# Kernel tuning notes

Hardware: AMD Instinct MI355X
Metric: run time of the kernel (lower is better)

Reference implementation:

```python
import jax, jax.numpy as jnp
import numpy as np

B, L, D, N = 4, 1024, 1024, 16
HD = D // N
DFF = 4 * D
EPS = 1e-5


def _ln(x, g, b):
    m = jnp.mean(x, axis=-1, keepdims=True)
    v = jnp.mean(jnp.square(x - m), axis=-1, keepdims=True)
    return (x - m) * jax.lax.rsqrt(v + EPS) * g + b


def setup_inputs() -> dict:
    key = jax.random.key(0)
    ks = jax.random.split(key, 8)
    s = 0.02
    return {
        "x": jax.random.normal(ks[0], (B, L, D), jnp.float32),
        "decay": jax.random.uniform(ks[1], (N, L, L), jnp.float32),
        "ln1_g": jnp.ones((D,), jnp.float32),
        "ln1_b": jnp.zeros((D,), jnp.float32),
        "proj_W": jax.random.normal(ks[2], (4 * D, D), jnp.float32) * s,
        "proj_b": jnp.zeros((4 * D,), jnp.float32),
        "reto_W": jax.random.normal(ks[3], (D, D), jnp.float32) * s,
        "reto_b": jnp.zeros((D,), jnp.float32),
        "ln2_g": jnp.ones((D,), jnp.float32),
        "ln2_b": jnp.zeros((D,), jnp.float32),
        "ffn1_W": jax.random.normal(ks[4], (DFF, D), jnp.float32) * s,
        "ffn1_b": jnp.zeros((DFF,), jnp.float32),
        "ffn2_W": jax.random.normal(ks[5], (D, DFF), jnp.float32) * s,
        "ffn2_b": jnp.zeros((D,), jnp.float32),
    }


def reference(x, decay, ln1_g, ln1_b, proj_W, proj_b, reto_W, reto_b,
              ln2_g, ln2_b, ffn1_W, ffn1_b, ffn2_W, ffn2_b):
    ln_x = _ln(x, ln1_g, ln1_b)
    p = ln_x @ proj_W.T + proj_b                      # [B, L, 4D]
    q, k, v, xo = jnp.split(p, 4, axis=-1)            # each [B, L, D]

    def heads(t):  # [B, L, D] -> [B, N, L, HD]
        return t.reshape(B, L, N, HD).transpose(0, 2, 1, 3)

    q, k, v = heads(q), heads(k), heads(v)
    scores = jnp.einsum('bnld,bnmd->bnlm', q, k) * decay[None]  # [B,N,L,L]
    ret = jnp.einsum('bnlm,bnmd->bnld', scores, v)              # [B,N,L,HD]
    ret = ret.transpose(0, 2, 1, 3).reshape(B, L, D)
    ret = ret * jax.nn.silu(xo)                                  # gated
    ret = ret @ reto_W.T + reto_b
    x = x + ret
    h = _ln(x, ln2_g, ln2_b)
    h = jax.nn.gelu(h @ ffn1_W.T + ffn1_b, approximate=False) @ ffn2_W.T + ffn2_b
    return x + h
```

## Files before the change

### kernel.cpp

```cpp
#include <hip/hip_runtime.h>


typedef _Float16 f16;
typedef _Float16 f16x8 __attribute__((ext_vector_type(8)));
typedef float floatx4 __attribute__((ext_vector_type(4)));

#define EP_BIAS_F16      0
#define EP_DECAY_F16     1
#define EP_BIAS_GELU_F16 2
#define EP_PARTIAL_F32   3

template <bool F32> struct out_sel { typedef f16 T; };
template <> struct out_sel<true>   { typedef float T; };

__device__ __forceinline__ void gload_lds16(const void* g, void* s) {
    __builtin_amdgcn_global_load_lds(
        (const __attribute__((address_space(1))) unsigned int*)g,
        (__attribute__((address_space(3))) unsigned int*)s, 16, 0, 0);
}

__device__ __forceinline__ float erf_fast(float x) {
    const float ax = fabsf(x);
    const float t  = __builtin_amdgcn_rcpf(1.f + 0.3275911f * ax);
    const float p  = t * (0.254829592f + t * (-0.284496736f + t * (1.421413741f +
                     t * (-1.453152027f + t * 1.061405429f))));
    const float r  = 1.f - p * __expf(-ax * ax);
    return copysignf(r, x);
}

__global__ __launch_bounds__(256, 4) void attn_fused(
    const f16* __restrict__ p, const f16* __restrict__ vT,
    const float* __restrict__ decay, f16* __restrict__ gated)
{
    const int z = blockIdx.y;
    const int b = z >> 4, h = z & 15;
    const int m0 = blockIdx.x * 64;

    __shared__ __align__(16) f16 Qs[64 * 64];
    __shared__ __align__(16) f16 Ks[64 * 64];
    __shared__ __align__(16) f16 Vs[64 * 64];
    __shared__ __align__(16) f16 Ss[64 * 72];

    const int t    = threadIdx.x;
    const int lane = t & 63;
    const int w    = t >> 6;
    const int quad = lane >> 4;
    const int fr   = lane & 15;
    const int wm   = (w >> 1) * 32;
    const int wn   = (w & 1) * 32;

    const f16*   Qg  = p + (size_t)(b * 1024 + m0) * 4096 + h * 64;
    const f16*   Kg  = p + (size_t)(b * 1024) * 4096 + 1024 + h * 64;
    const f16*   Vg  = vT + (size_t)z * 65536;
    const float* Dg  = decay + (size_t)h * 1048576 + (size_t)m0 * 1024;
    const f16*   XOg = p + (size_t)(b * 1024 + m0) * 4096 + 3072 + h * 64;

#pragma unroll
    for (int i = 0; i < 2; ++i) {
        const int ci = t + i * 256;
        const int r  = ci >> 3;
        const int c  = ((ci & 7) ^ (r & 7)) * 8;
        gload_lds16(Qg + (size_t)r * 4096 + c, &Qs[ci * 8]);
    }

    floatx4 o_acc[2][2] = {};

    for (int j = 0; j < 1024; j += 64) {
        float dreg[2][2][4];
#pragma unroll
        for (int tm = 0; tm < 2; ++tm)
#pragma unroll
            for (int tn = 0; tn < 2; ++tn)
#pragma unroll
                for (int r = 0; r < 4; ++r)
                    dreg[tm][tn][r] = Dg[(size_t)(wm + tm * 16 + quad * 4 + r) * 1024
                                          + j + wn + tn * 16 + fr];
#pragma unroll
        for (int i = 0; i < 2; ++i) {
            const int ci = t + i * 256;
            const int r  = ci >> 3;
            const int c  = ((ci & 7) ^ (r & 7)) * 8;
            gload_lds16(Kg + (size_t)(j + r) * 4096 + c, &Ks[ci * 8]);
        }
#pragma unroll
        for (int i = 0; i < 2; ++i) {
            const int ci = t + i * 256;
            const int r  = ci >> 3;
            const int c  = ((ci & 7) ^ (r & 7)) * 8;
            gload_lds16(Vg + (size_t)r * 1024 + j + c, &Vs[ci * 8]);
        }
        __syncthreads();

        floatx4 s_acc[2][2] = {};
#pragma unroll
        for (int kc = 0; kc < 2; ++kc) {
            const int cc = kc * 4 + quad;
            f16x8 af[2], bf[2];
#pragma unroll
            for (int tm = 0; tm < 2; ++tm) {
                const int q = wm + tm * 16 + fr;
                af[tm] = *(const f16x8*)&Qs[(q * 8 + (cc ^ (q & 7))) * 8];
            }
#pragma unroll
            for (int tn = 0; tn < 2; ++tn) {
                const int kv = wn + tn * 16 + fr;
                bf[tn] = *(const f16x8*)&Ks[(kv * 8 + (cc ^ (kv & 7))) * 8];
            }
#pragma unroll
            for (int tm = 0; tm < 2; ++tm)
#pragma unroll
                for (int tn = 0; tn < 2; ++tn)
                    s_acc[tm][tn] = __builtin_amdgcn_mfma_f32_16x16x32_f16(af[tm], bf[tn], s_acc[tm][tn], 0, 0, 0);
        }

#pragma unroll
        for (int tm = 0; tm < 2; ++tm)
#pragma unroll
            for (int tn = 0; tn < 2; ++tn)
#pragma unroll
                for (int r = 0; r < 4; ++r) {
                    const int q  = wm + tm * 16 + quad * 4 + r;
                    const int kv = wn + tn * 16 + fr;
                    Ss[q * 72 + kv] = (f16)(s_acc[tm][tn][r] * dreg[tm][tn][r]);
                }
        __syncthreads();

#pragma unroll
        for (int kc = 0; kc < 2; ++kc) {
            const int cc = kc * 4 + quad;
            f16x8 af[2], bf[2];
#pragma unroll
            for (int tm = 0; tm < 2; ++tm) {
                const int q = wm + tm * 16 + fr;
                af[tm] = *(const f16x8*)&Ss[q * 72 + cc * 8];
            }
#pragma unroll
            for (int tn = 0; tn < 2; ++tn) {
                const int d = wn + tn * 16 + fr;
                bf[tn] = *(const f16x8*)&Vs[(d * 8 + (cc ^ (d & 7))) * 8];
            }
#pragma unroll
            for (int tm = 0; tm < 2; ++tm)
#pragma unroll
                for (int tn = 0; tn < 2; ++tn)
                    o_acc[tm][tn] = __builtin_amdgcn_mfma_f32_16x16x32_f16(af[tm], bf[tn], o_acc[tm][tn], 0, 0, 0);
        }
        __syncthreads();
    }

#pragma unroll
    for (int tm = 0; tm < 2; ++tm)
#pragma unroll
        for (int tn = 0; tn < 2; ++tn)
#pragma unroll
            for (int r = 0; r < 4; ++r) {
                const int q = wm + tm * 16 + quad * 4 + r;
                const int d = wn + tn * 16 + fr;
                float g = (float)XOg[(size_t)q * 4096 + d];
                g = g * __builtin_amdgcn_rcpf(1.f + __expf(-g));
                Ss[q * 72 + d] = (f16)(o_acc[tm][tn][r] * g);
            }
    __syncthreads();
    f16* Og = gated + (size_t)(b * 1024 + m0) * 1024 + h * 64;
#pragma unroll
    for (int i = 0; i < 2; ++i) {
        const int jj = t + i * 256;
        const int rr = jj >> 3;
        const int cc = jj & 7;
        const uint2 lo = *(const uint2*)&Ss[rr * 72 + cc * 8];
        const uint2 hi = *(const uint2*)&Ss[rr * 72 + cc * 8 + 4];
        uint4 val = make_uint4(lo.x, lo.y, hi.x, hi.y);
        *(uint4*)(Og + (size_t)rr * 1024 + cc * 8) = val;
    }
}

template <int BM, int BN, int WM, int WN, int EP>
__global__ __launch_bounds__(256, 4) void gemm_bt(
    const f16* __restrict__ A, const f16* __restrict__ B, void* __restrict__ Cv,
    int M, int N, int K, int lda, int ldb, int ldc,
    long long sAo, long long sAi, long long sBo, long long sBi,
    long long sCo, long long sCi, int inner,
    int nsplit, int Kc, long long sCk,
    const float* __restrict__ bias,
    const void* __restrict__ aux, long long sXo, long long sXi, int ldaux)
{
    constexpr bool OUT_F32 = (EP == EP_PARTIAL_F32);
    typedef typename out_sel<OUT_F32>::T OutT;
    constexpr int ESIZE       = OUT_F32 ? 4 : 2;
    constexpr int CSTRIDE     = BN + 4;
    constexpr int TILE_BYTES  = (BM + BN) * 64 * 2;
    constexpr int STAGE_BYTES = BM * CSTRIDE * ESIZE;
    constexpr int SMEM_BYTES  = TILE_BYTES > STAGE_BYTES ? TILE_BYTES : STAGE_BYTES;

    __shared__ __align__(16) char smem[SMEM_BYTES];
    f16*  As = (f16*)smem;
    f16*  Bs = (f16*)(smem + BM * 128);
    OutT* Cs = (OutT*)smem;

    int z = blockIdx.z;
    const int ks = z % nsplit; z /= nsplit;
    const int zo = z / inner, zi = z % inner;
    A += zo * sAo + zi * sAi;
    B += zo * sBo + zi * sBi;
    const long long cOff = (long long)zo * sCo + (long long)zi * sCi + (long long)ks * sCk;
    const long long xOff = (long long)zo * sXo + (long long)zi * sXi;

    const int m0 = blockIdx.y * BM;
    const int n0 = blockIdx.x * BN;

    const int t    = threadIdx.x;
    const int lane = t & 63;
    const int w    = t >> 6;
    const int wm   = (w >> 1) * (WM * 16);
    const int wn   = (w & 1) * (WN * 16);
    const int fr   = lane & 15;
    const int quad = lane >> 4;

    constexpr int ACH = BM / 32;
    constexpr int BCH = BN / 32;

    floatx4 acc[WM][WN] = {};

    const int kbeg = ks * Kc, kend = kbeg + Kc;
    for (int kk = kbeg; kk < kend; kk += 64) {
#pragma unroll
        for (int i = 0; i < ACH; ++i) {
            const int ci = t + i * 256;
            const int r  = ci >> 3;
            const int c  = ((ci & 7) ^ (r & 7)) * 8;
            gload_lds16(A + (size_t)(m0 + r) * lda + kk + c, &As[ci * 8]);
        }
#pragma unroll
        for (int i = 0; i < BCH; ++i) {
            const int ci = t + i * 256;
            const int r  = ci >> 3;
            const int c  = ((ci & 7) ^ (r & 7)) * 8;
            gload_lds16(B + (size_t)(n0 + r) * ldb + kk + c, &Bs[ci * 8]);
        }
        __syncthreads();

#pragma unroll
        for (int kh = 0; kh < 2; ++kh) {
            const int cc = kh * 4 + quad;
            f16x8 af[WM], bf[WN];
#pragma unroll
            for (int tm = 0; tm < WM; ++tm) {
                const int r = wm + tm * 16 + fr;
                af[tm] = *(const f16x8*)&As[(r * 8 + (cc ^ (r & 7))) * 8];
            }
#pragma unroll
            for (int tn = 0; tn < WN; ++tn) {
                const int r = wn + tn * 16 + fr;
                bf[tn] = *(const f16x8*)&Bs[(r * 8 + (cc ^ (r & 7))) * 8];
            }
#pragma unroll
            for (int tm = 0; tm < WM; ++tm)
#pragma unroll
                for (int tn = 0; tn < WN; ++tn)
                    acc[tm][tn] = __builtin_amdgcn_mfma_f32_16x16x32_f16(af[tm], bf[tn], acc[tm][tn], 0, 0, 0);
        }
        __syncthreads();
    }

    const int er = quad * 4;
    const int ec = lane & 15;
#pragma unroll
    for (int tm = 0; tm < WM; ++tm) {
#pragma unroll
        for (int tn = 0; tn < WN; ++tn) {
#pragma unroll
            for (int r = 0; r < 4; ++r) {
                const int lrow = wm + tm * 16 + er + r;
                const int col  = wn + tn * 16 + ec;
                const int grow = m0 + lrow;
                const int gcol = n0 + col;
                const float v = acc[tm][tn][r];
                float val;
                if constexpr (EP == EP_BIAS_F16) {
                    val = v + bias[gcol];
                } else if constexpr (EP == EP_DECAY_F16) {
                    const float* dk = (const float*)aux + xOff;
                    val = v * dk[(size_t)grow * ldaux + gcol];
                } else if constexpr (EP == EP_BIAS_GELU_F16) {
                    const float u = v + bias[gcol];
                    val = 0.5f * u * (1.f + erf_fast(u * 0.70710678118f));
                } else {
                    val = v;
                }
                Cs[lrow * CSTRIDE + col] = (OutT)val;
            }
        }
    }
    __syncthreads();

    constexpr int PER_ROW = BN * ESIZE / 16;
    constexpr int NCHUNK  = (BM * PER_ROW) / 256;
#pragma unroll
    for (int i = 0; i < NCHUNK; ++i) {
        const int j  = t + i * 256;
        const int rr = j / PER_ROW;
        const int cc = j - rr * PER_ROW;
        const char* src = smem + (size_t)rr * (CSTRIDE * ESIZE) + (size_t)cc * 16;
        uint4 val;
        if constexpr (OUT_F32) {
            val = *(const uint4*)src;
        } else {
            const uint2 lo = *(const uint2*)src;
            const uint2 hi = *(const uint2*)(src + 8);
            val = make_uint4(lo.x, lo.y, hi.x, hi.y);
        }
        char* dst = (char*)Cv +
            (size_t)(cOff + (long long)(m0 + rr) * ldc + n0) * ESIZE +
            (size_t)cc * 16;
        *(uint4*)dst = val;
    }
}

__global__ __launch_bounds__(256) void reduce2_bias_res(
    const float4* __restrict__ P, const float* __restrict__ bias,
    const float4* __restrict__ res, float4* __restrict__ out)
{
    const int i = blockIdx.x * 256 + threadIdx.x;
    const int col4 = i & 255;
    const float4 a = P[i];
    const float4 b = P[i + 1048576];
    const float4 r = res[i];
    const float4 bi = ((const float4*)bias)[col4];
    float4 o;
    o.x = a.x + b.x + r.x + bi.x;
    o.y = a.y + b.y + r.y + bi.y;
    o.z = a.z + b.z + r.z + bi.z;
    o.w = a.w + b.w + r.w + bi.w;
    out[i] = o;
}

__global__ __launch_bounds__(256) void ln_to_f16(
    const float* __restrict__ x, const float* __restrict__ g,
    const float* __restrict__ b, f16* __restrict__ out)
{
    const int row = blockIdx.x;
    const int t = threadIdx.x;
    const float4 xv = ((const float4*)(x + (size_t)row * 1024))[t];
    float s  = xv.x + xv.y + xv.z + xv.w;
    float ss = xv.x * xv.x + xv.y * xv.y + xv.z * xv.z + xv.w * xv.w;
    for (int o = 32; o > 0; o >>= 1) {
        s  += __shfl_down(s, o, 64);
        ss += __shfl_down(ss, o, 64);
    }
    __shared__ float red[8];
    const int wv = t >> 6;
    if ((t & 63) == 0) { red[wv] = s; red[wv + 4] = ss; }
    __syncthreads();
    s  = red[0] + red[1] + red[2] + red[3];
    ss = red[4] + red[5] + red[6] + red[7];
    const float mean = s * (1.f / 1024.f);
    const float var  = ss * (1.f / 1024.f) - mean * mean;
    const float rstd = rsqrtf(var + 1e-5f);
    const float4 gv = ((const float4*)g)[t];
    const float4 bv = ((const float4*)b)[t];
    alignas(8) f16 h[4];
    h[0] = (f16)((xv.x - mean) * rstd * gv.x + bv.x);
    h[1] = (f16)((xv.y - mean) * rstd * gv.y + bv.y);
    h[2] = (f16)((xv.z - mean) * rstd * gv.z + bv.z);
    h[3] = (f16)((xv.w - mean) * rstd * gv.w + bv.w);
    ((uint2*)(out + (size_t)row * 1024))[t] = *(uint2*)h;
}

__global__ __launch_bounds__(256) void cast_f32_f16(
    const float* __restrict__ in, f16* __restrict__ out, int n4)
{
    const int i = blockIdx.x * 256 + threadIdx.x;
    if (i < n4) {
        const float4 v = ((const float4*)in)[i];
        alignas(8) f16 h[4] = {(f16)v.x, (f16)v.y, (f16)v.z, (f16)v.w};
        ((uint2*)out)[i] = *(uint2*)h;
    }
}

__global__ __launch_bounds__(256) void transpose_v(
    const f16* __restrict__ p, f16* __restrict__ vT)
{
    const int z = blockIdx.y;
    const int b = z >> 4, h = z & 15;
    const int m0 = blockIdx.x * 64;
    __shared__ f16 tile[64][72];
    const int t = threadIdx.x;
    const f16* src = p + (size_t)(b * 1024 + m0) * 4096 + 2048 + h * 64;
#pragma unroll
    for (int pass = 0; pass < 4; ++pass) {
        const int r = (t >> 4) + pass * 16;
        const int c = (t & 15) * 4;
        *(uint2*)&tile[r][c] = *(const uint2*)(src + (size_t)r * 4096 + c);
    }
    __syncthreads();
    f16* dst = vT + (size_t)z * 65536 + m0;
#pragma unroll
    for (int pass = 0; pass < 4; ++pass) {
        const int d  = (t >> 4) + pass * 16;
        const int mc = (t & 15) * 4;
        alignas(8) f16 tmp[4] = {tile[mc][d], tile[mc + 1][d], tile[mc + 2][d], tile[mc + 3][d]};
        *(uint2*)(dst + (size_t)d * 1024 + mc) = *(uint2*)tmp;
    }
}

extern "C" void kernel_launch(void* const* d_in, const int* in_sizes, int n_in,
                              void* d_out, int out_size, void* d_ws, size_t ws_size,
                              hipStream_t stream) {
    const float* x      = (const float*)d_in[0];
    const float* decay  = (const float*)d_in[1];
    const float* ln1_g  = (const float*)d_in[2];
    const float* ln1_b  = (const float*)d_in[3];
    const float* proj_W = (const float*)d_in[4];
    const float* proj_b = (const float*)d_in[5];
    const float* reto_W = (const float*)d_in[6];
    const float* reto_b = (const float*)d_in[7];
    const float* ln2_g  = (const float*)d_in[8];
    const float* ln2_b  = (const float*)d_in[9];
    const float* ffn1_W = (const float*)d_in[10];
    const float* ffn1_b = (const float*)d_in[11];
    const float* ffn2_W = (const float*)d_in[12];
    const float* ffn2_b = (const float*)d_in[13];
    float* out = (float*)d_out;

    char* w = (char*)d_ws;
    auto alloc = [&](size_t bytes) { char* r = w; w += (bytes + 255) & ~(size_t)255; return r; };
    f16*   Wp   = (f16*)alloc((size_t)4096 * 1024 * 2);
    f16*   Wr   = (f16*)alloc((size_t)1024 * 1024 * 2);
    f16*   W1   = (f16*)alloc((size_t)4096 * 1024 * 2);
    f16*   W2   = (f16*)alloc((size_t)1024 * 4096 * 2);
    f16*   buf8 = (f16*)alloc((size_t)4096 * 1024 * 2);
    f16*   p    = (f16*)alloc((size_t)4096 * 4096 * 2);
    f16*   S    = (f16*)alloc((size_t)16 * 1024 * 1024 * 2);
    float* y    = (float*)alloc((size_t)4096 * 1024 * 4);

    f16*   lnx   = buf8;
    f16*   vT    = buf8;
    f16*   hln   = buf8;
    f16*   gated = Wp;
    f16*   ffh   = p;
    float* Pk    = (float*)S;

    cast_f32_f16<<<4096, 256, 0, stream>>>(proj_W, Wp, 1048576);
    cast_f32_f16<<<1024, 256, 0, stream>>>(reto_W, Wr, 262144);
    cast_f32_f16<<<4096, 256, 0, stream>>>(ffn1_W, W1, 1048576);
    cast_f32_f16<<<4096, 256, 0, stream>>>(ffn2_W, W2, 1048576);

    ln_to_f16<<<4096, 256, 0, stream>>>(x, ln1_g, ln1_b, lnx);

    gemm_bt<128, 128, 4, 4, EP_BIAS_F16><<<dim3(32, 32, 1), 256, 0, stream>>>(
        lnx, Wp, p, 4096, 4096, 1024, 1024, 1024, 4096,
        0, 0, 0, 0, 0, 0, 1, 1, 1024, 0, proj_b, nullptr, 0, 0, 0);

    transpose_v<<<dim3(16, 64), 256, 0, stream>>>(p, vT);

    attn_fused<<<dim3(16, 64), 256, 0, stream>>>(p, vT, decay, gated);

    gemm_bt<128, 64, 4, 2, EP_PARTIAL_F32><<<dim3(16, 32, 2), 256, 0, stream>>>(
        gated, Wr, Pk, 4096, 1024, 1024, 1024, 1024, 1024,
        0, 0, 0, 0, 0, 0, 1, 2, 512, 4194304, nullptr, nullptr, 0, 0, 0);
    reduce2_bias_res<<<4096, 256, 0, stream>>>(
        (const float4*)Pk, reto_b, (const float4*)x, (float4*)y);

    ln_to_f16<<<4096, 256, 0, stream>>>(y, ln2_g, ln2_b, hln);

    gemm_bt<128, 128, 4, 4, EP_BIAS_GELU_F16><<<dim3(32, 32, 1), 256, 0, stream>>>(
        hln, W1, ffh, 4096, 4096, 1024, 1024, 1024, 4096,
        0, 0, 0, 0, 0, 0, 1, 1, 1024, 0, ffn1_b, nullptr, 0, 0, 0);

    gemm_bt<128, 64, 4, 2, EP_PARTIAL_F32><<<dim3(16, 32, 2), 256, 0, stream>>>(
        ffh, W2, Pk, 4096, 1024, 4096, 4096, 4096, 1024,
        0, 0, 0, 0, 0, 0, 1, 2, 2048, 4194304, nullptr, nullptr, 0, 0, 0);
    reduce2_bias_res<<<4096, 256, 0, stream>>>(
        (const float4*)Pk, ffn2_b, (const float4*)y, (float4*)out);
}
```

Before: 400.1 us.

## Process two batches per attention block to reuse decay tile loads

Each attention block now handles two batch elements for the same head and query tile, so every decay tile is read from global memory once and applied to both batches, halving decay traffic. Q fragments move from LDS into registers, loaded straight from global memory. K, V and S buffers are doubled, the grid is halved, and launch bounds drop to 2 blocks per CU, which lowers occupancy and raises register pressure.

Result: no change. 399.6 us (-0.1%).

```diff
diff --git a/kernel.cpp b/kernel.cpp
--- a/kernel.cpp
+++ b/kernel.cpp
@@ -28,18 +28,17 @@
     return copysignf(r, x);
 }
 
-__global__ __launch_bounds__(256, 4) void attn_fused(
+__global__ __launch_bounds__(256, 2) void attn_fused(
     const f16* __restrict__ p, const f16* __restrict__ vT,
     const float* __restrict__ decay, f16* __restrict__ gated)
 {
-    const int z = blockIdx.y;
-    const int b = z >> 4, h = z & 15;
+    const int y  = blockIdx.y;
+    const int bp = y >> 4, h = y & 15;
     const int m0 = blockIdx.x * 64;
 
-    __shared__ __align__(16) f16 Qs[64 * 64];
-    __shared__ __align__(16) f16 Ks[64 * 64];
-    __shared__ __align__(16) f16 Vs[64 * 64];
-    __shared__ __align__(16) f16 Ss[64 * 72];
+    __shared__ __align__(16) f16 Ks[2][64 * 64];
+    __shared__ __align__(16) f16 Vs[2][64 * 64];
+    __shared__ __align__(16) f16 Ss[2][64 * 72];
 
     const int t    = threadIdx.x;
     const int lane = t & 63;
@@ -49,21 +48,34 @@
     const int wm   = (w >> 1) * 32;
     const int wn   = (w & 1) * 32;
 
-    const f16*   Qg  = p + (size_t)(b * 1024 + m0) * 4096 + h * 64;
-    const f16*   Kg  = p + (size_t)(b * 1024) * 4096 + 1024 + h * 64;
-    const f16*   Vg  = vT + (size_t)z * 65536;
-    const float* Dg  = decay + (size_t)h * 1048576 + (size_t)m0 * 1024;
-    const f16*   XOg = p + (size_t)(b * 1024 + m0) * 4096 + 3072 + h * 64;
-
-#pragma unroll
-    for (int i = 0; i < 2; ++i) {
-        const int ci = t + i * 256;
-        const int r  = ci >> 3;
-        const int c  = ((ci & 7) ^ (r & 7)) * 8;
-        gload_lds16(Qg + (size_t)r * 4096 + c, &Qs[ci * 8]);
-    }
-
-    floatx4 o_acc[2][2] = {};
+    const f16* Qg[2];
+    const f16* Kg[2];
+    const f16* Vg[2];
+    const f16* XOg[2];
+#pragma unroll
+    for (int bi = 0; bi < 2; ++bi) {
+        const int b = bp * 2 + bi;
+        const int z = b * 16 + h;
+        Qg[bi]  = p + (size_t)(b * 1024 + m0) * 4096 + h * 64;
+        Kg[bi]  = p + (size_t)(b * 1024) * 4096 + 1024 + h * 64;
+        Vg[bi]  = vT + (size_t)z * 65536;
+        XOg[bi] = p + (size_t)(b * 1024 + m0) * 4096 + 3072 + h * 64;
+    }
+    const float* Dg = decay + (size_t)h * 1048576 + (size_t)m0 * 1024;
+
+    f16x8 qreg[2][2][2];
+#pragma unroll
+    for (int bi = 0; bi < 2; ++bi)
+#pragma unroll
+        for (int tm = 0; tm < 2; ++tm)
+#pragma unroll
+            for (int kc = 0; kc < 2; ++kc) {
+                const int q  = wm + tm * 16 + fr;
+                const int cc = kc * 4 + quad;
+                qreg[bi][tm][kc] = *(const f16x8*)(Qg[bi] + (size_t)q * 4096 + cc * 8);
+            }
+
+    floatx4 o_acc[2][2][2] = {};
 
     for (int j = 0; j < 1024; j += 64) {
         float dreg[2][2][4];
@@ -80,97 +92,100 @@
             const int ci = t + i * 256;
             const int r  = ci >> 3;
             const int c  = ((ci & 7) ^ (r & 7)) * 8;
-            gload_lds16(Kg + (size_t)(j + r) * 4096 + c, &Ks[ci * 8]);
-        }
+            gload_lds16(Kg[0] + (size_t)(j + r) * 4096 + c, &Ks[0][ci * 8]);
+            gload_lds16(Kg[1] + (size_t)(j + r) * 4096 + c, &Ks[1][ci * 8]);
+            gload_lds16(Vg[0] + (size_t)r * 1024 + j + c, &Vs[0][ci * 8]);
+            gload_lds16(Vg[1] + (size_t)r * 1024 + j + c, &Vs[1][ci * 8]);
+        }
+        __syncthreads();
+
+#pragma unroll
+        for (int bi = 0; bi < 2; ++bi) {
+            floatx4 s_acc[2][2] = {};
+#pragma unroll
+            for (int kc = 0; kc < 2; ++kc) {
+                const int cc = kc * 4 + quad;
+                f16x8 bf[2];
+#pragma unroll
+                for (int tn = 0; tn < 2; ++tn) {
+                    const int kv = wn + tn * 16 + fr;
+                    bf[tn] = *(const f16x8*)&Ks[bi][(kv * 8 + (cc ^ (kv & 7))) * 8];
+                }
+#pragma unroll
+                for (int tm = 0; tm < 2; ++tm)
+#pragma unroll
+                    for (int tn = 0; tn < 2; ++tn)
+                        s_acc[tm][tn] = __builtin_amdgcn_mfma_f32_16x16x32_f16(
+                            qreg[bi][tm][kc], bf[tn], s_acc[tm][tn], 0, 0, 0);
+            }
+#pragma unroll
+            for (int tm = 0; tm < 2; ++tm)
+#pragma unroll
+                for (int tn = 0; tn < 2; ++tn)
+#pragma unroll
+                    for (int r = 0; r < 4; ++r) {
+                        const int q  = wm + tm * 16 + quad * 4 + r;
+                        const int kv = wn + tn * 16 + fr;
+                        Ss[bi][q * 72 + kv] = (f16)(s_acc[tm][tn][r] * dreg[tm][tn][r]);
+                    }
+        }
+        __syncthreads();
+
+#pragma unroll
+        for (int bi = 0; bi < 2; ++bi) {
+#pragma unroll
+            for (int kc = 0; kc < 2; ++kc) {
+                const int cc = kc * 4 + quad;
+                f16x8 af[2], bf[2];
+#pragma unroll
+                for (int tm = 0; tm < 2; ++tm) {
+                    const int q = wm + tm * 16 + fr;
+                    af[tm] = *(const f16x8*)&Ss[bi][q * 72 + cc * 8];
+                }
+#pragma unroll
+                for (int tn = 0; tn < 2; ++tn) {
+                    const int d = wn + tn * 16 + fr;
+                    bf[tn] = *(const f16x8*)&Vs[bi][(d * 8 + (cc ^ (d & 7))) * 8];
+                }
+#pragma unroll
+                for (int tm = 0; tm < 2; ++tm)
+#pragma unroll
+                    for (int tn = 0; tn < 2; ++tn)
+                        o_acc[bi][tm][tn] = __builtin_amdgcn_mfma_f32_16x16x32_f16(
+                            af[tm], bf[tn], o_acc[bi][tm][tn], 0, 0, 0);
+            }
+        }
+        __syncthreads();
+    }
+
+#pragma unroll
+    for (int bi = 0; bi < 2; ++bi)
+#pragma unroll
+        for (int tm = 0; tm < 2; ++tm)
+#pragma unroll
+            for (int tn = 0; tn < 2; ++tn)
+#pragma unroll
+                for (int r = 0; r < 4; ++r) {
+                    const int q = wm + tm * 16 + quad * 4 + r;
+                    const int d = wn + tn * 16 + fr;
+                    float g = (float)XOg[bi][(size_t)q * 4096 + d];
+                    g = g * __builtin_amdgcn_rcpf(1.f + __expf(-g));
+                    Ss[bi][q * 72 + d] = (f16)(o_acc[bi][tm][tn][r] * g);
+                }
+    __syncthreads();
+#pragma unroll
+    for (int bi = 0; bi < 2; ++bi) {
+        f16* Og = gated + (size_t)((bp * 2 + bi) * 1024 + m0) * 1024 + h * 64;
 #pragma unroll
         for (int i = 0; i < 2; ++i) {
-            const int ci = t + i * 256;
-            const int r  = ci >> 3;
-            const int c  = ((ci & 7) ^ (r & 7)) * 8;
-            gload_lds16(Vg + (size_t)r * 1024 + j + c, &Vs[ci * 8]);
-        }
-        __syncthreads();
-
-        floatx4 s_acc[2][2] = {};
-#pragma unroll
-        for (int kc = 0; kc < 2; ++kc) {
-            const int cc = kc * 4 + quad;
-            f16x8 af[2], bf[2];
-#pragma unroll
-            for (int tm = 0; tm < 2; ++tm) {
-                const int q = wm + tm * 16 + fr;
-                af[tm] = *(const f16x8*)&Qs[(q * 8 + (cc ^ (q & 7))) * 8];
-            }
-#pragma unroll
-            for (int tn = 0; tn < 2; ++tn) {
-                const int kv = wn + tn * 16 + fr;
-                bf[tn] = *(const f16x8*)&Ks[(kv * 8 + (cc ^ (kv & 7))) * 8];
-            }
-#pragma unroll
-            for (int tm = 0; tm < 2; ++tm)
-#pragma unroll
-                for (int tn = 0; tn < 2; ++tn)
-                    s_acc[tm][tn] = __builtin_amdgcn_mfma_f32_16x16x32_f16(af[tm], bf[tn], s_acc[tm][tn], 0, 0, 0);
-        }
-
-#pragma unroll
-        for (int tm = 0; tm < 2; ++tm)
-#pragma unroll
-            for (int tn = 0; tn < 2; ++tn)
-#pragma unroll
-                for (int r = 0; r < 4; ++r) {
-                    const int q  = wm + tm * 16 + quad * 4 + r;
-                    const int kv = wn + tn * 16 + fr;
-                    Ss[q * 72 + kv] = (f16)(s_acc[tm][tn][r] * dreg[tm][tn][r]);
-                }
-        __syncthreads();
-
-#pragma unroll
-        for (int kc = 0; kc < 2; ++kc) {
-            const int cc = kc * 4 + quad;
-            f16x8 af[2], bf[2];
-#pragma unroll
-            for (int tm = 0; tm < 2; ++tm) {
-                const int q = wm + tm * 16 + fr;
-                af[tm] = *(const f16x8*)&Ss[q * 72 + cc * 8];
-            }
-#pragma unroll
-            for (int tn = 0; tn < 2; ++tn) {
-                const int d = wn + tn * 16 + fr;
-                bf[tn] = *(const f16x8*)&Vs[(d * 8 + (cc ^ (d & 7))) * 8];
-            }
-#pragma unroll
-            for (int tm = 0; tm < 2; ++tm)
-#pragma unroll
-                for (int tn = 0; tn < 2; ++tn)
-                    o_acc[tm][tn] = __builtin_amdgcn_mfma_f32_16x16x32_f16(af[tm], bf[tn], o_acc[tm][tn], 0, 0, 0);
-        }
-        __syncthreads();
-    }
-
-#pragma unroll
-    for (int tm = 0; tm < 2; ++tm)
-#pragma unroll
-        for (int tn = 0; tn < 2; ++tn)
-#pragma unroll
-            for (int r = 0; r < 4; ++r) {
-                const int q = wm + tm * 16 + quad * 4 + r;
-                const int d = wn + tn * 16 + fr;
-                float g = (float)XOg[(size_t)q * 4096 + d];
-                g = g * __builtin_amdgcn_rcpf(1.f + __expf(-g));
-                Ss[q * 72 + d] = (f16)(o_acc[tm][tn][r] * g);
-            }
-    __syncthreads();
-    f16* Og = gated + (size_t)(b * 1024 + m0) * 1024 + h * 64;
-#pragma unroll
-    for (int i = 0; i < 2; ++i) {
-        const int jj = t + i * 256;
-        const int rr = jj >> 3;
-        const int cc = jj & 7;
-        const uint2 lo = *(const uint2*)&Ss[rr * 72 + cc * 8];
-        const uint2 hi = *(const uint2*)&Ss[rr * 72 + cc * 8 + 4];
-        uint4 val = make_uint4(lo.x, lo.y, hi.x, hi.y);
-        *(uint4*)(Og + (size_t)rr * 1024 + cc * 8) = val;
+            const int jj = t + i * 256;
+            const int rr = jj >> 3;
+            const int cc = jj & 7;
+            const uint2 lo = *(const uint2*)&Ss[bi][rr * 72 + cc * 8];
+            const uint2 hi = *(const uint2*)&Ss[bi][rr * 72 + cc * 8 + 4];
+            uint4 val = make_uint4(lo.x, lo.y, hi.x, hi.y);
+            *(uint4*)(Og + (size_t)rr * 1024 + cc * 8) = val;
+        }
     }
 }
 
@@ -453,7 +468,7 @@
 
     transpose_v<<<dim3(16, 64), 256, 0, stream>>>(p, vT);
 
-    attn_fused<<<dim3(16, 64), 256, 0, stream>>>(p, vT, decay, gated);
+    attn_fused<<<dim3(16, 32), 256, 0, stream>>>(p, vT, decay, gated);
 
     gemm_bt<128, 64, 4, 2, EP_PARTIAL_F32><<<dim3(16, 32, 2), 256, 0, stream>>>(
         gated, Wr, Pk, 4096, 1024, 1024, 1024, 1024, 1024,
```

## Restructure retention attention to share decay tiles across batch pairs with double buffering

Applied to the files above, without the earlier changes.

Each attention block now handles two batches for the same head and query tile, so every decay tile loaded from global memory is reused for both batches. This halves decay traffic, which is the largest input at 64 MB in fp32. K/V tiles are double-buffered in LDS, alternating between the two batches. Q is kept in registers. Each wave owns 16 query rows with a private score buffer, which removes one block-wide barrier per step. The cost is higher register pressure (occupancy hint lowered to 2) and half as many blocks, which reduces parallelism.

Measured after the change: 410.4 us. 1.03x slower.

```diff
diff --git a/kernel.cpp b/kernel.cpp
--- a/kernel.cpp
+++ b/kernel.cpp
@@ -28,150 +28,151 @@
     return copysignf(r, x);
 }
 
-__global__ __launch_bounds__(256, 4) void attn_fused(
+__global__ __launch_bounds__(256, 2) void attn_fused(
     const f16* __restrict__ p, const f16* __restrict__ vT,
     const float* __restrict__ decay, f16* __restrict__ gated)
 {
-    const int z = blockIdx.y;
-    const int b = z >> 4, h = z & 15;
+    const int y  = blockIdx.y;
+    const int bp = y >> 4, h = y & 15;
     const int m0 = blockIdx.x * 64;
 
-    __shared__ __align__(16) f16 Qs[64 * 64];
-    __shared__ __align__(16) f16 Ks[64 * 64];
-    __shared__ __align__(16) f16 Vs[64 * 64];
-    __shared__ __align__(16) f16 Ss[64 * 72];
+    __shared__ __align__(16) f16 Kb[2][64 * 64];
+    __shared__ __align__(16) f16 Vb[2][64 * 64];
+    __shared__ __align__(16) f16 Ss[4][16 * 68];
 
     const int t    = threadIdx.x;
     const int lane = t & 63;
     const int w    = t >> 6;
     const int quad = lane >> 4;
     const int fr   = lane & 15;
-    const int wm   = (w >> 1) * 32;
-    const int wn   = (w & 1) * 32;
-
-    const f16*   Qg  = p + (size_t)(b * 1024 + m0) * 4096 + h * 64;
-    const f16*   Kg  = p + (size_t)(b * 1024) * 4096 + 1024 + h * 64;
-    const f16*   Vg  = vT + (size_t)z * 65536;
+    const int wq0  = w * 16;
+
+    const int b0 = bp * 2, b1 = b0 + 1;
+    const f16*   Qg0 = p + (size_t)(b0 * 1024 + m0) * 4096 + h * 64;
+    const f16*   Qg1 = p + (size_t)(b1 * 1024 + m0) * 4096 + h * 64;
+    const f16*   Kg0 = p + (size_t)(b0 * 1024) * 4096 + 1024 + h * 64;
+    const f16*   Kg1 = p + (size_t)(b1 * 1024) * 4096 + 1024 + h * 64;
+    const f16*   Vg0 = vT + (size_t)(b0 * 16 + h) * 65536;
+    const f16*   Vg1 = vT + (size_t)(b1 * 16 + h) * 65536;
+    const f16*   XOg0 = p + (size_t)(b0 * 1024 + m0) * 4096 + 3072 + h * 64;
+    const f16*   XOg1 = p + (size_t)(b1 * 1024 + m0) * 4096 + 3072 + h * 64;
     const float* Dg  = decay + (size_t)h * 1048576 + (size_t)m0 * 1024;
-    const f16*   XOg = p + (size_t)(b * 1024 + m0) * 4096 + 3072 + h * 64;
-
-#pragma unroll
-    for (int i = 0; i < 2; ++i) {
-        const int ci = t + i * 256;
-        const int r  = ci >> 3;
-        const int c  = ((ci & 7) ^ (r & 7)) * 8;
-        gload_lds16(Qg + (size_t)r * 4096 + c, &Qs[ci * 8]);
-    }
-
-    floatx4 o_acc[2][2] = {};
-
-    for (int j = 0; j < 1024; j += 64) {
-        float dreg[2][2][4];
-#pragma unroll
-        for (int tm = 0; tm < 2; ++tm)
-#pragma unroll
-            for (int tn = 0; tn < 2; ++tn)
-#pragma unroll
-                for (int r = 0; r < 4; ++r)
-                    dreg[tm][tn][r] = Dg[(size_t)(wm + tm * 16 + quad * 4 + r) * 1024
-                                          + j + wn + tn * 16 + fr];
-#pragma unroll
-        for (int i = 0; i < 2; ++i) {
-            const int ci = t + i * 256;
-            const int r  = ci >> 3;
-            const int c  = ((ci & 7) ^ (r & 7)) * 8;
-            gload_lds16(Kg + (size_t)(j + r) * 4096 + c, &Ks[ci * 8]);
-        }
-#pragma unroll
-        for (int i = 0; i < 2; ++i) {
-            const int ci = t + i * 256;
-            const int r  = ci >> 3;
-            const int c  = ((ci & 7) ^ (r & 7)) * 8;
-            gload_lds16(Vg + (size_t)r * 1024 + j + c, &Vs[ci * 8]);
-        }
-        __syncthreads();
-
-        floatx4 s_acc[2][2] = {};
-#pragma unroll
-        for (int kc = 0; kc < 2; ++kc) {
-            const int cc = kc * 4 + quad;
-            f16x8 af[2], bf[2];
-#pragma unroll
-            for (int tm = 0; tm < 2; ++tm) {
-                const int q = wm + tm * 16 + fr;
-                af[tm] = *(const f16x8*)&Qs[(q * 8 + (cc ^ (q & 7))) * 8];
-            }
-#pragma unroll
-            for (int tn = 0; tn < 2; ++tn) {
-                const int kv = wn + tn * 16 + fr;
-                bf[tn] = *(const f16x8*)&Ks[(kv * 8 + (cc ^ (kv & 7))) * 8];
-            }
-#pragma unroll
-            for (int tm = 0; tm < 2; ++tm)
-#pragma unroll
-                for (int tn = 0; tn < 2; ++tn)
-                    s_acc[tm][tn] = __builtin_amdgcn_mfma_f32_16x16x32_f16(af[tm], bf[tn], s_acc[tm][tn], 0, 0, 0);
-        }
-
-#pragma unroll
-        for (int tm = 0; tm < 2; ++tm)
-#pragma unroll
-            for (int tn = 0; tn < 2; ++tn)
-#pragma unroll
-                for (int r = 0; r < 4; ++r) {
-                    const int q  = wm + tm * 16 + quad * 4 + r;
-                    const int kv = wn + tn * 16 + fr;
-                    Ss[q * 72 + kv] = (f16)(s_acc[tm][tn][r] * dreg[tm][tn][r]);
-                }
-        __syncthreads();
-
-#pragma unroll
-        for (int kc = 0; kc < 2; ++kc) {
-            const int cc = kc * 4 + quad;
-            f16x8 af[2], bf[2];
-#pragma unroll
-            for (int tm = 0; tm < 2; ++tm) {
-                const int q = wm + tm * 16 + fr;
-                af[tm] = *(const f16x8*)&Ss[q * 72 + cc * 8];
-            }
-#pragma unroll
-            for (int tn = 0; tn < 2; ++tn) {
-                const int d = wn + tn * 16 + fr;
-                bf[tn] = *(const f16x8*)&Vs[(d * 8 + (cc ^ (d & 7))) * 8];
-            }
-#pragma unroll
-            for (int tm = 0; tm < 2; ++tm)
-#pragma unroll
-                for (int tn = 0; tn < 2; ++tn)
-                    o_acc[tm][tn] = __builtin_amdgcn_mfma_f32_16x16x32_f16(af[tm], bf[tn], o_acc[tm][tn], 0, 0, 0);
-        }
-        __syncthreads();
-    }
-
-#pragma unroll
-    for (int tm = 0; tm < 2; ++tm)
-#pragma unroll
-        for (int tn = 0; tn < 2; ++tn)
-#pragma unroll
-            for (int r = 0; r < 4; ++r) {
-                const int q = wm + tm * 16 + quad * 4 + r;
-                const int d = wn + tn * 16 + fr;
-                float g = (float)XOg[(size_t)q * 4096 + d];
-                g = g * __builtin_amdgcn_rcpf(1.f + __expf(-g));
-                Ss[q * 72 + d] = (f16)(o_acc[tm][tn][r] * g);
-            }
+
+    f16x8 q00, q01, q10, q11;
+    {
+        const size_t qrow = (size_t)(wq0 + fr) * 4096;
+        q00 = *(const f16x8*)(Qg0 + qrow + (0 * 4 + quad) * 8);
+        q01 = *(const f16x8*)(Qg0 + qrow + (1 * 4 + quad) * 8);
+        q10 = *(const f16x8*)(Qg1 + qrow + (0 * 4 + quad) * 8);
+        q11 = *(const f16x8*)(Qg1 + qrow + (1 * 4 + quad) * 8);
+    }
+
+    floatx4 oa0[4] = {}, oa1[4] = {};
+    float dA[16], dB[16];
+
+    const float* Dt = Dg + (size_t)(wq0 + quad * 4) * 1024 + fr;
+
+#define DLOAD(dst, jj) { _Pragma("unroll") \
+    for (int tn = 0; tn < 4; ++tn) { _Pragma("unroll") \
+      for (int r = 0; r < 4; ++r) \
+        dst[tn * 4 + r] = Dt[(size_t)r * 1024 + (jj) + tn * 16]; } }
+
+#define STAGE(Kgp, Vgp, jj, pb) { _Pragma("unroll") \
+    for (int i = 0; i < 2; ++i) { \
+      const int ci = t + i * 256; \
+      const int r  = ci >> 3; \
+      const int c  = ((ci & 7) ^ (r & 7)) * 8; \
+      gload_lds16((Kgp) + (size_t)((jj) + r) * 4096 + c, &Kb[pb][ci * 8]); \
+      gload_lds16((Vgp) + (size_t)r * 1024 + (jj) + c, &Vb[pb][ci * 8]); \
+    } }
+
+#define STEP(qa, qb, oa, dreg, pb) { \
+    floatx4 sa[4] = {}; \
+    _Pragma("unroll") \
+    for (int kc = 0; kc < 2; ++kc) { \
+      const int cc = kc * 4 + quad; \
+      f16x8 bf[4]; \
+      _Pragma("unroll") \
+      for (int tn = 0; tn < 4; ++tn) { \
+        const int kv = tn * 16 + fr; \
+        bf[tn] = *(const f16x8*)&Kb[pb][(kv * 8 + (cc ^ (kv & 7))) * 8]; \
+      } \
+      _Pragma("unroll") \
+      for (int tn = 0; tn < 4; ++tn) \
+        sa[tn] = __builtin_amdgcn_mfma_f32_16x16x32_f16(kc ? (qb) : (qa), bf[tn], sa[tn], 0, 0, 0); \
+    } \
+    _Pragma("unroll") \
+    for (int tn = 0; tn < 4; ++tn) { _Pragma("unroll") \
+      for (int r = 0; r < 4; ++r) \
+        Ss[w][(quad * 4 + r) * 68 + tn * 16 + fr] = (f16)(sa[tn][r] * dreg[tn * 4 + r]); } \
+    _Pragma("unroll") \
+    for (int kc = 0; kc < 2; ++kc) { \
+      const int cc = kc * 4 + quad; \
+      const f16x8 af = *(const f16x8*)&Ss[w][fr * 68 + cc * 8]; \
+      f16x8 bf[4]; \
+      _Pragma("unroll") \
+      for (int tn = 0; tn < 4; ++tn) { \
+        const int d = tn * 16 + fr; \
+        bf[tn] = *(const f16x8*)&Vb[pb][(d * 8 + (cc ^ (d & 7))) * 8]; \
+      } \
+      _Pragma("unroll") \
+      for (int tn = 0; tn < 4; ++tn) \
+        oa[tn] = __builtin_amdgcn_mfma_f32_16x16x32_f16(af, bf[tn], oa[tn], 0, 0, 0); \
+    } }
+
+#define EPILOG(oa, XOgp, bq) { \
+    _Pragma("unroll") \
+    for (int tn = 0; tn < 4; ++tn) { _Pragma("unroll") \
+      for (int r = 0; r < 4; ++r) { \
+        const int qrow = wq0 + quad * 4 + r; \
+        const int d = tn * 16 + fr; \
+        float g = (float)XOgp[(size_t)qrow * 4096 + d]; \
+        g = g * __builtin_amdgcn_rcpf(1.f + __expf(-g)); \
+        Ss[w][(quad * 4 + r) * 68 + tn * 16 + fr] = (f16)(oa[tn][r] * g); \
+      } } \
+    f16* Og = gated + (size_t)((bq) * 1024 + m0 + wq0) * 1024 + h * 64; \
+    _Pragma("unroll") \
+    for (int i = 0; i < 2; ++i) { \
+      const int jj = lane + i * 64; \
+      const int rr = jj >> 3; \
+      const int cc = jj & 7; \
+      const uint2 lo = *(const uint2*)&Ss[w][rr * 68 + cc * 8]; \
+      const uint2 hi = *(const uint2*)&Ss[w][rr * 68 + cc * 8 + 4]; \
+      uint4 val = make_uint4(lo.x, lo.y, hi.x, hi.y); \
+      *(uint4*)(Og + (size_t)rr * 1024 + cc * 8) = val; \
+    } }
+
+    STAGE(Kg0, Vg0, 0, 0);
+    DLOAD(dA, 0);
     __syncthreads();
-    f16* Og = gated + (size_t)(b * 1024 + m0) * 1024 + h * 64;
-#pragma unroll
-    for (int i = 0; i < 2; ++i) {
-        const int jj = t + i * 256;
-        const int rr = jj >> 3;
-        const int cc = jj & 7;
-        const uint2 lo = *(const uint2*)&Ss[rr * 72 + cc * 8];
-        const uint2 hi = *(const uint2*)&Ss[rr * 72 + cc * 8 + 4];
-        uint4 val = make_uint4(lo.x, lo.y, hi.x, hi.y);
-        *(uint4*)(Og + (size_t)rr * 1024 + cc * 8) = val;
-    }
+
+    for (int tt = 0; tt < 16; tt += 2) {
+        const int j0 = tt << 6;
+        STAGE(Kg1, Vg1, j0, 1);
+        STEP(q00, q01, oa0, dA, 0);
+        __syncthreads();
+        STAGE(Kg0, Vg0, j0 + 64, 0);
+        DLOAD(dB, j0 + 64);
+        STEP(q10, q11, oa1, dA, 1);
+        __syncthreads();
+        STAGE(Kg1, Vg1, j0 + 64, 1);
+        STEP(q00, q01, oa0, dB, 0);
+        __syncthreads();
+        if (tt < 14) {
+            STAGE(Kg0, Vg0, j0 + 128, 0);
+            DLOAD(dA, j0 + 128);
+        }
+        STEP(q10, q11, oa1, dB, 1);
+        __syncthreads();
+    }
+
+    EPILOG(oa0, XOg0, b0);
+    EPILOG(oa1, XOg1, b1);
+
+#undef DLOAD
+#undef STAGE
+#undef STEP
+#undef EPILOG
 }
 
 template <int BM, int BN, int WM, int WN, int EP>
@@ -453,7 +454,7 @@
 
     transpose_v<<<dim3(16, 64), 256, 0, stream>>>(p, vT);
 
-    attn_fused<<<dim3(16, 64), 256, 0, stream>>>(p, vT, decay, gated);
+    attn_fused<<<dim3(16, 32), 256, 0, stream>>>(p, vT, decay, gated);
 
     gemm_bt<128, 64, 4, 2, EP_PARTIAL_F32><<<dim3(16, 32, 2), 256, 0, stream>>>(
         gated, Wr, Pk, 4096, 1024, 1024, 1024, 1024, 1024,
```
